# Kernel tuning notes

Measured on AMD Instinct MI355X. Metric: run time of the kernel, lower is better.

## Reference

```python
import jax, jax.numpy as jnp
import numpy as np

N_AGENTS = 8
STATE_DIM = 256
EMBED_DIM = 32
BATCH = 65536


def setup_inputs() -> dict:
    key = jax.random.key(0)
    ks = jax.random.split(key, 12)
    s = 1.0 / np.sqrt(STATE_DIM)
    se = 1.0 / np.sqrt(EMBED_DIM)
    return {
        "agent_qs": jax.random.normal(ks[0], (BATCH, N_AGENTS), dtype=jnp.float32),
        "states": jax.random.normal(ks[1], (BATCH, STATE_DIM), dtype=jnp.float32),
        # hyper_w_1: Linear(state_dim, embed_dim * n_agents)
        "w1_W": jax.random.uniform(ks[2], (STATE_DIM, EMBED_DIM * N_AGENTS), jnp.float32, -s, s),
        "w1_b": jax.random.uniform(ks[3], (EMBED_DIM * N_AGENTS,), jnp.float32, -s, s),
        # hyper_w_final: Linear(state_dim, embed_dim)
        "wf_W": jax.random.uniform(ks[4], (STATE_DIM, EMBED_DIM), jnp.float32, -s, s),
        "wf_b": jax.random.uniform(ks[5], (EMBED_DIM,), jnp.float32, -s, s),
        # hyper_b_1: Linear(state_dim, embed_dim)
        "b1_W": jax.random.uniform(ks[6], (STATE_DIM, EMBED_DIM), jnp.float32, -s, s),
        "b1_b": jax.random.uniform(ks[7], (EMBED_DIM,), jnp.float32, -s, s),
        # V: Linear(state_dim, embed_dim) -> ReLU -> Linear(embed_dim, 1)
        "v1_W": jax.random.uniform(ks[8], (STATE_DIM, EMBED_DIM), jnp.float32, -s, s),
        "v1_b": jax.random.uniform(ks[9], (EMBED_DIM,), jnp.float32, -s, s),
        "v2_W": jax.random.uniform(ks[10], (EMBED_DIM, 1), jnp.float32, -se, se),
        "v2_b": jax.random.uniform(ks[11], (1,), jnp.float32, -se, se),
    }


def reference(agent_qs, states, w1_W, w1_b, wf_W, wf_b, b1_W, b1_b, v1_W, v1_b, v2_W, v2_b):
    B = agent_qs.shape[0]
    # hypernet weights (abs for monotonicity)
    w1 = jnp.abs(states @ w1_W + w1_b).reshape(B, N_AGENTS, EMBED_DIM)   # [B, A, E]
    w_final = jnp.abs(states @ wf_W + wf_b)                               # [B, E]
    b1 = states @ b1_W + b1_b                                             # [B, E]
    # hidden = elu(agent_qs^T w1 + b1): [B,1,A] @ [B,A,E] -> [B,E]
    hidden = jax.nn.elu(jnp.einsum("ba,bae->be", agent_qs, w1) + b1)
    # mixed = hidden @ w_final: [B,1,E] @ [B,E,1] -> [B,1]
    mixed = jnp.sum(hidden * w_final, axis=-1, keepdims=True)             # [B, 1]
    # state value V(s)
    state_value = jax.nn.relu(states @ v1_W + v1_b) @ v2_W + v2_b         # [B, 1]
    return mixed + state_value
```

## Files before the change

kernel.cpp:

```cpp
#include <hip/hip_runtime.h>
#include <math.h>


#define NTILES 22
#define KCHUNKS 8
#define LDS_SLOTS 128

typedef __attribute__((ext_vector_type(8))) short short8;
typedef __attribute__((ext_vector_type(4))) float float4v;

__device__ __forceinline__ unsigned short f2b(float f) {
    unsigned int u = __float_as_uint(f);
    u = u + 0x7fffu + ((u >> 16) & 1u);
    return (unsigned short)(u >> 16);
}

__device__ __forceinline__ void gl2lds16(const unsigned short* g, unsigned short* l) {
    __builtin_amdgcn_global_load_lds(
        (const __attribute__((address_space(1))) unsigned int*)g,
        (__attribute__((address_space(3))) unsigned int*)l,
        16, 0, 0);
}

__global__ void repack_b(const float* __restrict__ w1_W,
                         const float* __restrict__ wf_W,
                         const float* __restrict__ b1_W,
                         const float* __restrict__ v1_W,
                         unsigned short* __restrict__ brep) {
    int idx = blockIdx.x * 256 + threadIdx.x;
    int lane = idx & 63;
    int slot = idx >> 6;
    int t, kc;
    if (slot < 128) { t = slot >> 3; kc = slot & 7; }
    else            { int r = slot - 128; kc = r / 6; t = 16 + r % 6; }
    int kbase = kc * 32 + (lane >> 4) * 8;
    int n = t * 16 + (lane & 15);
    short8 frag;
#pragma unroll
    for (int j = 0; j < 8; ++j) {
        int k = kbase + j;
        float val;
        if (n < 256)      val = w1_W[k * 256 + n];
        else if (n < 288) val = wf_W[k * 32 + (n - 256)];
        else if (n < 320) val = b1_W[k * 32 + (n - 288)];
        else              val = v1_W[k * 32 + (n - 320)];
        frag[j] = (short)f2b(val);
    }
    *(short8*)(&brep[idx * 8]) = frag;
}

__global__ void __launch_bounds__(512, 1)
qmix_main(const float* __restrict__ agent_qs,
          const float* __restrict__ states,
          const unsigned short* __restrict__ brep,
          const float* __restrict__ w1_b,
          const float* __restrict__ wf_b,
          const float* __restrict__ b1_b,
          const float* __restrict__ v1_b,
          const float* __restrict__ v2_W,
          const float* __restrict__ v2_b,
          float* __restrict__ out) {
    __shared__ __align__(16) unsigned short wlds[LDS_SLOTS * 64 * 8];

    const int tid  = threadIdx.x;
    const int wave = tid >> 6, lane = tid & 63;
    const int quad = lane >> 4, l16 = lane & 15;
    const int r0 = blockIdx.x * 256 + wave * 32 + l16;
    const float* srow0 = states + (size_t)r0 * 256;
    const float* srow1 = srow0 + 16 * 256;

    for (int s = wave; s < LDS_SLOTS; s += 8)
        gl2lds16(brep + (size_t)(s * 64 + lane) * 8, wlds + s * 512);

    float4v s0a = *(const float4v*)(srow0 + quad * 8);
    float4v s0b = *(const float4v*)(srow0 + quad * 8 + 4);
    float4v s1a = *(const float4v*)(srow1 + quad * 8);
    float4v s1b = *(const float4v*)(srow1 + quad * 8 + 4);

    float4v acc[2][NTILES];
#pragma unroll
    for (int g = 0; g < 2; ++g)
#pragma unroll
        for (int t = 0; t < NTILES; ++t)
#pragma unroll
            for (int q = 0; q < 4; ++q) acc[g][t][q] = 0.f;

    __syncthreads();

    const short8* wl = (const short8*)wlds + lane;
    const short8* ws = (const short8*)brep + LDS_SLOTS * 64 + lane;

    for (int kc = 0; kc < KCHUNKS; ++kc) {
        short8 sf[6];
#pragma unroll
        for (int u = 0; u < 6; ++u) sf[u] = ws[(kc * 6 + u) * 64];
        short8 b0, b1;
#pragma unroll
        for (int j = 0; j < 4; ++j) {
            b0[j] = (short)f2b(s0a[j]); b0[4 + j] = (short)f2b(s0b[j]);
            b1[j] = (short)f2b(s1a[j]); b1[4 + j] = (short)f2b(s1b[j]);
        }
        if (kc < KCHUNKS - 1) {
            const float* p0 = srow0 + (kc + 1) * 32 + quad * 8;
            const float* p1 = srow1 + (kc + 1) * 32 + quad * 8;
            s0a = *(const float4v*)(p0);
            s0b = *(const float4v*)(p0 + 4);
            s1a = *(const float4v*)(p1);
            s1b = *(const float4v*)(p1 + 4);
        }
#pragma unroll
        for (int t = 0; t < 16; ++t) {
            short8 af = wl[(t * 8 + kc) * 64];
            acc[0][t] = __builtin_amdgcn_mfma_f32_16x16x32_bf16(af, b0, acc[0][t], 0, 0, 0);
            acc[1][t] = __builtin_amdgcn_mfma_f32_16x16x32_bf16(af, b1, acc[1][t], 0, 0, 0);
        }
#pragma unroll
        for (int u = 0; u < 6; ++u) {
            acc[0][16 + u] = __builtin_amdgcn_mfma_f32_16x16x32_bf16(sf[u], b0, acc[0][16 + u], 0, 0, 0);
            acc[1][16 + u] = __builtin_amdgcn_mfma_f32_16x16x32_bf16(sf[u], b1, acc[1][16 + u], 0, 0, 0);
        }
    }

#pragma unroll
    for (int g = 0; g < 2; ++g) {
        const int row = r0 + g * 16;
        float4v q0 = *(const float4v*)(agent_qs + (size_t)row * 8);
        float4v q1 = *(const float4v*)(agent_qs + (size_t)row * 8 + 4);
        float qv[8] = {q0[0], q0[1], q0[2], q0[3], q1[0], q1[1], q1[2], q1[3]};

        float qacc[8], wfv[8], b1v[8], svp = 0.f;
#pragma unroll
        for (int s = 0; s < 8; ++s) qacc[s] = 0.f;

#pragma unroll
        for (int t = 0; t < NTILES; ++t) {
            const float* bptr =
                (t < 16) ? (w1_b + t * 16) :
                (t < 18) ? (wf_b + (t - 16) * 16) :
                (t < 20) ? (b1_b + (t - 18) * 16) : (v1_b + (t - 20) * 16);
            float4v bb = *(const float4v*)(bptr + quad * 4);
            float vb[4];
#pragma unroll
            for (int j = 0; j < 4; ++j) vb[j] = acc[g][t][j] + bb[j];

            if (t < 16) {
                float q = qv[t >> 1];
                int base = (t & 1) * 4;
#pragma unroll
                for (int j = 0; j < 4; ++j) qacc[base + j] += q * fabsf(vb[j]);
            } else if (t < 18) {
                int base = (t - 16) * 4;
#pragma unroll
                for (int j = 0; j < 4; ++j) wfv[base + j] = fabsf(vb[j]);
            } else if (t < 20) {
                int base = (t - 18) * 4;
#pragma unroll
                for (int j = 0; j < 4; ++j) b1v[base + j] = vb[j];
            } else {
                int ebase = (t - 20) * 16 + quad * 4;
#pragma unroll
                for (int j = 0; j < 4; ++j)
                    svp += fmaxf(vb[j], 0.f) * v2_W[ebase + j];
            }
        }

        float mix = 0.f;
#pragma unroll
        for (int s = 0; s < 8; ++s) {
            float h = qacc[s] + b1v[s];
            h = h > 0.f ? h : (__expf(h) - 1.f);
            mix += h * wfv[s];
        }
        float tot = mix + svp;
        tot += __shfl_xor(tot, 16);
        tot += __shfl_xor(tot, 32);
        if (quad == 0) out[row] = tot + v2_b[0];
    }
}

extern "C" void kernel_launch(void* const* d_in, const int* in_sizes, int n_in,
                              void* d_out, int out_size, void* d_ws, size_t ws_size,
                              hipStream_t stream) {
    const float* agent_qs = (const float*)d_in[0];
    const float* states   = (const float*)d_in[1];
    const float* w1_W = (const float*)d_in[2];
    const float* w1_b = (const float*)d_in[3];
    const float* wf_W = (const float*)d_in[4];
    const float* wf_b = (const float*)d_in[5];
    const float* b1_W = (const float*)d_in[6];
    const float* b1_b = (const float*)d_in[7];
    const float* v1_W = (const float*)d_in[8];
    const float* v1_b = (const float*)d_in[9];
    const float* v2_W = (const float*)d_in[10];
    const float* v2_b = (const float*)d_in[11];
    float* out = (float*)d_out;
    unsigned short* brep = (unsigned short*)d_ws;

    repack_b<<<44, 256, 0, stream>>>(w1_W, wf_W, b1_W, v1_W, brep);
    qmix_main<<<256, 512, 0, stream>>>(agent_qs, states, brep,
                                       w1_b, wf_b, b1_b, v1_b, v2_W, v2_b, out);
}
```

Baseline: 158.3 us.

## Halve block size, loop two row tiles per block, deepen prefetch of states and weights

Blocks drop from 512 to 256 threads (4 waves), and each block now handles its 256 rows as two sequential 128-row tiles. The LDS weight load is shared across both tiles. The k-loop is fully unrolled, with a 3-deep register ring prefetching states two chunks ahead and double-buffered global weight fragments. The aim is to hide global load latency better, at the cost of fewer waves per CU for latency hiding and higher register pressure.

Measured after the change: 246.2 us. 1.56x slower.

```diff
diff --git a/kernel.cpp b/kernel.cpp
--- a/kernel.cpp
+++ b/kernel.cpp
@@ -49,7 +49,7 @@
     *(short8*)(&brep[idx * 8]) = frag;
 }
 
-__global__ void __launch_bounds__(512, 1)
+__global__ void __launch_bounds__(256, 1)
 qmix_main(const float* __restrict__ agent_qs,
           const float* __restrict__ states,
           const unsigned short* __restrict__ brep,
@@ -60,121 +60,135 @@
           const float* __restrict__ v2_W,
           const float* __restrict__ v2_b,
           float* __restrict__ out) {
-    __shared__ __align__(16) unsigned short wlds[LDS_SLOTS * 64 * 8];
+    __shared__ __align__(16) unsigned short wlds[LDS_SLOTS * 512];
 
     const int tid  = threadIdx.x;
     const int wave = tid >> 6, lane = tid & 63;
     const int quad = lane >> 4, l16 = lane & 15;
-    const int r0 = blockIdx.x * 256 + wave * 32 + l16;
-    const float* srow0 = states + (size_t)r0 * 256;
-    const float* srow1 = srow0 + 16 * 256;
-
-    for (int s = wave; s < LDS_SLOTS; s += 8)
+
+    for (int s = wave; s < LDS_SLOTS; s += 4)
         gl2lds16(brep + (size_t)(s * 64 + lane) * 8, wlds + s * 512);
-
-    float4v s0a = *(const float4v*)(srow0 + quad * 8);
-    float4v s0b = *(const float4v*)(srow0 + quad * 8 + 4);
-    float4v s1a = *(const float4v*)(srow1 + quad * 8);
-    float4v s1b = *(const float4v*)(srow1 + quad * 8 + 4);
-
-    float4v acc[2][NTILES];
-#pragma unroll
-    for (int g = 0; g < 2; ++g)
-#pragma unroll
-        for (int t = 0; t < NTILES; ++t)
-#pragma unroll
-            for (int q = 0; q < 4; ++q) acc[g][t][q] = 0.f;
-
     __syncthreads();
 
     const short8* wl = (const short8*)wlds + lane;
     const short8* ws = (const short8*)brep + LDS_SLOTS * 64 + lane;
 
-    for (int kc = 0; kc < KCHUNKS; ++kc) {
-        short8 sf[6];
-#pragma unroll
-        for (int u = 0; u < 6; ++u) sf[u] = ws[(kc * 6 + u) * 64];
-        short8 b0, b1;
-#pragma unroll
-        for (int j = 0; j < 4; ++j) {
-            b0[j] = (short)f2b(s0a[j]); b0[4 + j] = (short)f2b(s0b[j]);
-            b1[j] = (short)f2b(s1a[j]); b1[4 + j] = (short)f2b(s1b[j]);
+    for (int tile = 0; tile < 2; ++tile) {
+        const int r0 = blockIdx.x * 256 + tile * 128 + wave * 32 + l16;
+        const float* srow0 = states + (size_t)r0 * 256;
+        const float* srow1 = srow0 + 16 * 256;
+
+        float4v st[2][3][2];
+#pragma unroll
+        for (int r = 0; r < 2; ++r) {
+            st[0][r][0] = *(const float4v*)(srow0 + r * 32 + quad * 8);
+            st[0][r][1] = *(const float4v*)(srow0 + r * 32 + quad * 8 + 4);
+            st[1][r][0] = *(const float4v*)(srow1 + r * 32 + quad * 8);
+            st[1][r][1] = *(const float4v*)(srow1 + r * 32 + quad * 8 + 4);
         }
-        if (kc < KCHUNKS - 1) {
-            const float* p0 = srow0 + (kc + 1) * 32 + quad * 8;
-            const float* p1 = srow1 + (kc + 1) * 32 + quad * 8;
-            s0a = *(const float4v*)(p0);
-            s0b = *(const float4v*)(p0 + 4);
-            s1a = *(const float4v*)(p1);
-            s1b = *(const float4v*)(p1 + 4);
+        short8 sf[2][6];
+#pragma unroll
+        for (int u = 0; u < 6; ++u) sf[0][u] = ws[u * 64];
+
+        float4v acc[2][NTILES];
+#pragma unroll
+        for (int g = 0; g < 2; ++g)
+#pragma unroll
+            for (int t = 0; t < NTILES; ++t)
+#pragma unroll
+                for (int q = 0; q < 4; ++q) acc[g][t][q] = 0.f;
+
+#pragma unroll
+        for (int kc = 0; kc < KCHUNKS; ++kc) {
+            if (kc + 2 < KCHUNKS) {
+                int r = (kc + 2) % 3;
+                st[0][r][0] = *(const float4v*)(srow0 + (kc + 2) * 32 + quad * 8);
+                st[0][r][1] = *(const float4v*)(srow0 + (kc + 2) * 32 + quad * 8 + 4);
+                st[1][r][0] = *(const float4v*)(srow1 + (kc + 2) * 32 + quad * 8);
+                st[1][r][1] = *(const float4v*)(srow1 + (kc + 2) * 32 + quad * 8 + 4);
+            }
+            if (kc + 1 < KCHUNKS) {
+#pragma unroll
+                for (int u = 0; u < 6; ++u)
+                    sf[(kc + 1) & 1][u] = ws[((kc + 1) * 6 + u) * 64];
+            }
+            short8 b0, b1;
+            {
+                int r = kc % 3;
+#pragma unroll
+                for (int j = 0; j < 4; ++j) {
+                    b0[j] = (short)f2b(st[0][r][0][j]); b0[4 + j] = (short)f2b(st[0][r][1][j]);
+                    b1[j] = (short)f2b(st[1][r][0][j]); b1[4 + j] = (short)f2b(st[1][r][1][j]);
+                }
+            }
+#pragma unroll
+            for (int t = 0; t < 16; ++t) {
+                short8 af = wl[(t * 8 + kc) * 64];
+                acc[0][t] = __builtin_amdgcn_mfma_f32_16x16x32_bf16(af, b0, acc[0][t], 0, 0, 0);
+                acc[1][t] = __builtin_amdgcn_mfma_f32_16x16x32_bf16(af, b1, acc[1][t], 0, 0, 0);
+            }
+#pragma unroll
+            for (int u = 0; u < 6; ++u) {
+                acc[0][16 + u] = __builtin_amdgcn_mfma_f32_16x16x32_bf16(sf[kc & 1][u], b0, acc[0][16 + u], 0, 0, 0);
+                acc[1][16 + u] = __builtin_amdgcn_mfma_f32_16x16x32_bf16(sf[kc & 1][u], b1, acc[1][16 + u], 0, 0, 0);
+            }
         }
-#pragma unroll
-        for (int t = 0; t < 16; ++t) {
-            short8 af = wl[(t * 8 + kc) * 64];
-            acc[0][t] = __builtin_amdgcn_mfma_f32_16x16x32_bf16(af, b0, acc[0][t], 0, 0, 0);
-            acc[1][t] = __builtin_amdgcn_mfma_f32_16x16x32_bf16(af, b1, acc[1][t], 0, 0, 0);
+
+#pragma unroll
+        for (int g = 0; g < 2; ++g) {
+            const int row = r0 + g * 16;
+            float4v q0 = *(const float4v*)(agent_qs + (size_t)row * 8);
+            float4v q1 = *(const float4v*)(agent_qs + (size_t)row * 8 + 4);
+            float qv[8] = {q0[0], q0[1], q0[2], q0[3], q1[0], q1[1], q1[2], q1[3]};
+
+            float qacc[8], wfv[8], b1v[8], svp = 0.f;
+#pragma unroll
+            for (int s = 0; s < 8; ++s) qacc[s] = 0.f;
+
+#pragma unroll
+            for (int t = 0; t < NTILES; ++t) {
+                const float* bptr =
+                    (t < 16) ? (w1_b + t * 16) :
+                    (t < 18) ? (wf_b + (t - 16) * 16) :
+                    (t < 20) ? (b1_b + (t - 18) * 16) : (v1_b + (t - 20) * 16);
+                float4v bb = *(const float4v*)(bptr + quad * 4);
+                float vb[4];
+#pragma unroll
+                for (int j = 0; j < 4; ++j) vb[j] = acc[g][t][j] + bb[j];
+
+                if (t < 16) {
+                    float q = qv[t >> 1];
+                    int base = (t & 1) * 4;
+#pragma unroll
+                    for (int j = 0; j < 4; ++j) qacc[base + j] += q * fabsf(vb[j]);
+                } else if (t < 18) {
+                    int base = (t - 16) * 4;
+#pragma unroll
+                    for (int j = 0; j < 4; ++j) wfv[base + j] = fabsf(vb[j]);
+                } else if (t < 20) {
+                    int base = (t - 18) * 4;
+#pragma unroll
+                    for (int j = 0; j < 4; ++j) b1v[base + j] = vb[j];
+                } else {
+                    int ebase = (t - 20) * 16 + quad * 4;
+#pragma unroll
+                    for (int j = 0; j < 4; ++j)
+                        svp += fmaxf(vb[j], 0.f) * v2_W[ebase + j];
+                }
+            }
+
+            float mix = 0.f;
+#pragma unroll
+            for (int s = 0; s < 8; ++s) {
+                float h = qacc[s] + b1v[s];
+                h = h > 0.f ? h : (__expf(h) - 1.f);
+                mix += h * wfv[s];
+            }
+            float tot = mix + svp;
+            tot += __shfl_xor(tot, 16);
+            tot += __shfl_xor(tot, 32);
+            if (quad == 0) out[row] = tot + v2_b[0];
         }
-#pragma unroll
-        for (int u = 0; u < 6; ++u) {
-            acc[0][16 + u] = __builtin_amdgcn_mfma_f32_16x16x32_bf16(sf[u], b0, acc[0][16 + u], 0, 0, 0);
-            acc[1][16 + u] = __builtin_amdgcn_mfma_f32_16x16x32_bf16(sf[u], b1, acc[1][16 + u], 0, 0, 0);
-        }
-    }
-
-#pragma unroll
-    for (int g = 0; g < 2; ++g) {
-        const int row = r0 + g * 16;
-        float4v q0 = *(const float4v*)(agent_qs + (size_t)row * 8);
-        float4v q1 = *(const float4v*)(agent_qs + (size_t)row * 8 + 4);
-        float qv[8] = {q0[0], q0[1], q0[2], q0[3], q1[0], q1[1], q1[2], q1[3]};
-
-        float qacc[8], wfv[8], b1v[8], svp = 0.f;
-#pragma unroll
-        for (int s = 0; s < 8; ++s) qacc[s] = 0.f;
-
-#pragma unroll
-        for (int t = 0; t < NTILES; ++t) {
-            const float* bptr =
-                (t < 16) ? (w1_b + t * 16) :
-                (t < 18) ? (wf_b + (t - 16) * 16) :
-                (t < 20) ? (b1_b + (t - 18) * 16) : (v1_b + (t - 20) * 16);
-            float4v bb = *(const float4v*)(bptr + quad * 4);
-            float vb[4];
-#pragma unroll
-            for (int j = 0; j < 4; ++j) vb[j] = acc[g][t][j] + bb[j];
-
-            if (t < 16) {
-                float q = qv[t >> 1];
-                int base = (t & 1) * 4;
-#pragma unroll
-                for (int j = 0; j < 4; ++j) qacc[base + j] += q * fabsf(vb[j]);
-            } else if (t < 18) {
-                int base = (t - 16) * 4;
-#pragma unroll
-                for (int j = 0; j < 4; ++j) wfv[base + j] = fabsf(vb[j]);
-            } else if (t < 20) {
-                int base = (t - 18) * 4;
-#pragma unroll
-                for (int j = 0; j < 4; ++j) b1v[base + j] = vb[j];
-            } else {
-                int ebase = (t - 20) * 16 + quad * 4;
-#pragma unroll
-                for (int j = 0; j < 4; ++j)
-                    svp += fmaxf(vb[j], 0.f) * v2_W[ebase + j];
-            }
-        }
-
-        float mix = 0.f;
-#pragma unroll
-        for (int s = 0; s < 8; ++s) {
-            float h = qacc[s] + b1v[s];
-            h = h > 0.f ? h : (__expf(h) - 1.f);
-            mix += h * wfv[s];
-        }
-        float tot = mix + svp;
-        tot += __shfl_xor(tot, 16);
-        tot += __shfl_xor(tot, 32);
-        if (quad == 0) out[row] = tot + v2_b[0];
     }
 }
 
@@ -197,6 +211,6 @@
     unsigned short* brep = (unsigned short*)d_ws;
 
     repack_b<<<44, 256, 0, stream>>>(w1_W, wf_W, b1_W, v1_W, brep);
-    qmix_main<<<256, 512, 0, stream>>>(agent_qs, states, brep,
+    qmix_main<<<256, 256, 0, stream>>>(agent_qs, states, brep,
                                        w1_b, wf_b, b1_b, v1_b, v2_W, v2_b, out);
 }
```
